# Kernel tuning notes

Measured on AMD Instinct MI355X. Metric: run time of the kernel, lower is better.

## Reference

```python
import jax, jax.numpy as jnp
import numpy as np
from jax.scipy.special import i0

# NUFFT adjoint (gridding) configuration, matching m_op.plan(uv, (256,256), (512,512), (6,6))
N = 256          # image side
K = 512
J = 6            # kernel support per dim
B = 8            # batch
M = 100000       # n_measurements
ALPHA = K / N    # oversampling = 2
BETA = float(np.pi * np.sqrt((J / ALPHA * (ALPHA - 0.5)) ** 2 - 0.8))  # Fessler KB beta


def setup_inputs() -> dict:
    key = jax.random.key(0)
    k1, k2, k3, k4 = jax.random.split(key, 4)
    y_real = jax.random.normal(k1, (B, M), dtype=jnp.float32)
    y_imag = jax.random.normal(k2, (B, M), dtype=jnp.float32)
    weights = jax.random.uniform(k3, (M,), dtype=jnp.float32, minval=0.1, maxval=1.0)
    uv = jax.random.uniform(k4, (M, 2), dtype=jnp.float32,
                            minval=-np.pi, maxval=np.pi)
    return {"y_real": y_real, "y_imag": y_imag, "weights": weights, "uv": uv}


def _kb(t):
    # Kaiser-Bessel interpolation kernel, support |t| <= J/2
    u = 2.0 * t / J
    return i0(BETA * jnp.sqrt(jnp.clip(1.0 - u * u, 0.0))) / i0(jnp.asarray(BETA, jnp.float32))


def reference(y_real, y_imag, weights, uv):
    # weighted complex measurements: inputs * measurement_weights
    y = (y_real + 1j * y_imag) * weights[None, :]           # (B, M) complex64

    # map uv in [-pi, pi) to oversampled grid coords in [0, K)
    kf = uv * (K / (2.0 * np.pi))                            # (M, 2), DC at index 0 (mod K)
    base = jnp.floor(kf).astype(jnp.int32)                   # (M, 2)
    offs = jnp.arange(-J // 2 + 1, J // 2 + 1)               # [-2..3], 6 taps
    idx = base[:, :, None] + offs[None, None, :]             # (M, 2, J)
    dist = idx.astype(jnp.float32) - kf[:, :, None]
    w = _kb(dist)                                            # (M, 2, J) separable weights
    idxm = jnp.mod(idx, K)                                   # wrap onto torus

    w2 = (w[:, 0, :, None] * w[:, 1, None, :]).reshape(M, J * J)          # (M, 36)
    lin = (idxm[:, 0, :, None] * K + idxm[:, 1, None, :]).reshape(M * J * J)
    vals = (y[:, :, None] * w2[None, :, :].astype(jnp.complex64)).reshape(B, M * J * J)

    # scatter-add onto oversampled Fourier grid
    grid = jnp.zeros((B, K * K), jnp.complex64).at[:, lin].add(vals)
    grid = grid.reshape(B, K, K)

    # inverse FFT, center, crop to N x N
    img = jnp.fft.fftshift(jnp.fft.ifft2(grid), axes=(1, 2))
    c = K // 2
    img = img[:, c - N // 2:c + N // 2, c - N // 2:c + N // 2]

    # deapodization: divide by 1D FT of the KB kernel (always real here since BETA > pi*J/4*... )
    n = jnp.arange(N, dtype=jnp.float32) - N // 2
    xf = np.pi * J * n / K
    arg = BETA * BETA - xf * xf
    d = jnp.sinh(jnp.sqrt(arg)) / jnp.sqrt(arg)              # (N,)
    apod = d[:, None] * d[None, :]

    x = (jnp.real(img) / apod).astype(jnp.float32)           # tf.math.real(adj_op(...))

    # per-image min-max rescale
    tmax = jnp.max(x, axis=(1, 2), keepdims=True)
    tmin = jnp.min(x, axis=(1, 2), keepdims=True)
    return (x - tmin) / (tmax - tmin)
```

## Files before the change

### kernel.cpp

```cpp
#include <hip/hip_runtime.h>
#include <math.h>

#define NN 256
#define KK 512
#define JJ 6
#define BB 8
#define MPTS 100000
#define NBINS (KK * KK)
#define KF_SCALE 81.48733086305615f

typedef _Float16 h8 __attribute__((ext_vector_type(8)));
typedef _Float16 h2 __attribute__((ext_vector_type(2)));


__device__ __forceinline__ float i0f_dev(float x) {
    float ax = fabsf(x);
    if (ax < 3.75f) {
        float t = x / 3.75f; t *= t;
        return 1.0f + t*(3.5156229f + t*(3.0899424f + t*(1.2067492f +
               t*(0.2659732f + t*(0.0360768f + t*0.0045813f)))));
    } else {
        float t = 3.75f / ax;
        return (expf(ax) * rsqrtf(ax)) *
               (0.39894228f + t*(0.01328592f + t*(0.00225319f + t*(-0.00157565f +
                t*(0.00916281f + t*(-0.02057706f + t*(0.02635537f +
                t*(-0.01647633f + t*0.00392377f))))))));
    }
}

__device__ __forceinline__ float kbf(float t, float beta, float inv_i0b) {
    float u = t * (1.0f / 3.0f);
    float q = fmaxf(1.0f - u * u, 0.0f);
    return i0f_dev(beta * sqrtf(q)) * inv_i0b;
}

__device__ __forceinline__ int wave_scan(int x, int lane) {
#pragma unroll
    for (int off = 1; off < 64; off <<= 1) {
        int y = __shfl_up(x, off, 64);
        if (lane >= off) x += y;
    }
    return x;
}

__device__ __forceinline__ void build_row_prefix(const int* __restrict__ btot,
                                                 int* sPref, int t)
{
    if (t < 64) {
        int carry = 0;
        if (t == 0) sPref[0] = 0;
#pragma unroll
        for (int k = 0; k < 8; ++k) {
            int x = btot[k * 64 + t];
            int incl = wave_scan(x, t);
            sPref[k * 64 + t + 1] = incl + carry;
            carry += __shfl(incl, 63, 64);
        }
    }
}

__device__ __forceinline__ float kb_lut(const float* __restrict__ sT, float t) {
    float u = (t + 3.0f) * (1023.0f / 6.0f);
    int i = (int)u;
    i = min(i, 1022);
    float f = u - (float)i;
    float a = sT[i];
    return a + f * (sT[i + 1] - sT[i]);
}

__device__ __forceinline__ void tw_lookup(const float* __restrict__ twc,
                                          const float* __restrict__ tws,
                                          int idx, float& wr, float& wi) {
    float sg = (idx & 256) ? -1.0f : 1.0f;
    int ib = idx & 255;
    wr = sg * twc[ib];
    wi = sg * tws[ib];
}


__device__ __forceinline__ void fill_point(
    const float2* __restrict__ uv2,
    const float* __restrict__ y_real, const float* __restrict__ y_imag,
    const float* __restrict__ weights, const int* __restrict__ offsets,
    const int* sPref,
    int* counts, char* rec, const float* sT, int m)
{
    float2 u = uv2[m];
    float kf0 = u.x * KF_SCALE;
    float kf1 = u.y * KF_SCALE;
    float f0 = floorf(kf0), f1 = floorf(kf1);
    float fr0 = kf0 - f0, fr1 = kf1 - f1;
    int b0r = (int)f0 & (KK - 1);
    int b1c = (int)f1 & (KK - 1);
    int bin = (b0r << 9) | b1c;
    int old = atomicSub(&counts[bin], 1);
    int slot = sPref[b0r] + offsets[bin] + old - 1;

    _Float16 hw[12];
#pragma unroll
    for (int j = 0; j < JJ; ++j) {
        hw[j]     = (_Float16)kb_lut(sT, (float)(j - 2) - fr0);
        hw[6 + j] = (_Float16)kb_lut(sT, (float)(j - 2) - fr1);
    }

    float4 c0v, c1v;
    _Float16* p0 = (_Float16*)&c0v;
    _Float16* p1 = (_Float16*)&c1v;
#pragma unroll
    for (int j = 0; j < 8; ++j) p0[j] = hw[j];
#pragma unroll
    for (int j = 0; j < 4; ++j) p1[j] = hw[8 + j];
    ((int*)&c1v)[2] = b1c;
    ((int*)&c1v)[3] = 0;

    float wm = weights[m];
    h8 ha, hb;
#pragma unroll
    for (int b = 0; b < 4; ++b) {
        ha[2 * b]     = (_Float16)(y_real[b * MPTS + m] * wm);
        ha[2 * b + 1] = (_Float16)(y_imag[b * MPTS + m] * wm);
        hb[2 * b]     = (_Float16)(y_real[(b + 4) * MPTS + m] * wm);
        hb[2 * b + 1] = (_Float16)(y_imag[(b + 4) * MPTS + m] * wm);
    }

    float4* dst = (float4*)(rec + (size_t)slot * 64);
    dst[0] = c0v;
    dst[1] = c1v;
    dst[2] = *(float4*)&ha;
    dst[3] = *(float4*)&hb;
}

__device__ __forceinline__ void gather_strip(
    const int* __restrict__ offsets, const int* sPref,
    const char* __restrict__ rec,
    h2* __restrict__ gridh, int j, int w, int lane)
{
    int half = lane >> 5;
    int l32 = lane & 31;
    int xcd = j & 7;
    int c0 = (xcd << 6) + ((j >> 3) & 63);
    int q4 = j >> 9;
    int c1base = (q4 << 7) + (w << 5);
    int c1 = c1base + l32;

    float aR[4], aI[4];
#pragma unroll
    for (int b = 0; b < 4; ++b) { aR[b] = 0.0f; aI[b] = 0.0f; }

    for (int j0 = 0; j0 < JJ; ++j0) {
        int r0 = (c0 - (j0 - 2)) & (KK - 1);
        int rowbase = r0 << 9;
        int P = sPref[r0];
        int rowEnd = sPref[r0 + 1];

        int li = min(lane, 37);
        int vec = offsets[rowbase + ((c1base - 3 + li) & 511)];

        int ps = P + __shfl(vec, l32, 64);
#pragma unroll
        for (int d = 0; d < 6; ++d) {
            int b1 = (c1 - 3 + d) & 511;
            int nxt = P + __shfl(vec, l32 + d + 1, 64);
            int pe = (b1 == 511) ? rowEnd : nxt;
            for (int p = ps; p < pe; ++p) {
                const char* rp = rec + (size_t)p * 64;
                float w0 = (float)*(const _Float16*)(rp + j0 * 2);
                float w1 = (float)*(const _Float16*)(rp + 12 + (5 - d) * 2);
                float ww = w0 * w1;
                h8 yv = *(const h8*)(rp + 32 + (half << 4));
#pragma unroll
                for (int b = 0; b < 4; ++b) {
                    aR[b] += (float)yv[2 * b]     * ww;
                    aI[b] += (float)yv[2 * b + 1] * ww;
                }
            }
            ps = nxt;
        }
    }

    int c = (c0 << 9) + c1;
#pragma unroll
    for (int b = 0; b < 4; ++b) {
        h2 v;
        v[0] = (_Float16)aR[b];
        v[1] = (_Float16)aI[b];
        gridh[((size_t)((half << 2) + b) << 18) + c] = v;
    }
}

__device__ __forceinline__ void wave_fft512(float xr[8], float xi[8], int lane,
                                            const float* __restrict__ twc,
                                            const float* __restrict__ tws)
{
    float a0r = xr[0]+xr[4], a0i = xi[0]+xi[4];
    float a4r = xr[0]-xr[4], a4i = xi[0]-xi[4];
    float a2r = xr[2]+xr[6], a2i = xi[2]+xi[6];
    float a6r = xr[2]-xr[6], a6i = xi[2]-xi[6];
    float a1r = xr[1]+xr[5], a1i = xi[1]+xi[5];
    float a5r = xr[1]-xr[5], a5i = xi[1]-xi[5];
    float a3r = xr[3]+xr[7], a3i = xi[3]+xi[7];
    float a7r = xr[3]-xr[7], a7i = xi[3]-xi[7];
    float b0r = a0r+a2r, b0i = a0i+a2i;
    float b2r = a0r-a2r, b2i = a0i-a2i;
    float b4r = a4r-a6i, b4i = a4i+a6r;
    float b6r = a4r+a6i, b6i = a4i-a6r;
    float b1r = a1r+a3r, b1i = a1i+a3i;
    float b3r = a1r-a3r, b3i = a1i-a3i;
    float b5r = a5r-a7i, b5i = a5i+a7r;
    float b7r = a5r+a7i, b7i = a5i-a7r;
    const float S2 = 0.70710678118654752f;
    float w5r = S2*(b5r-b5i), w5i = S2*(b5r+b5i);
    float w7r = -S2*(b7r+b7i), w7i = S2*(b7r-b7i);
    float y1r = b4r+w5r, y1i = b4i+w5i;
    float y5r = b4r-w5r, y5i = b4i-w5i;
    float y2r = b2r-b3i, y2i = b2i+b3r;
    float y6r = b2r+b3i, y6i = b2i-b3r;
    float y3r = b6r+w7r, y3i = b6i+w7i;
    float y7r = b6r-w7r, y7i = b6i-w7i;

    int p = __brev((unsigned)lane) >> 26;
    xr[0] = b0r+b1r; xi[0] = b0i+b1i;
    {
        float wr, wi;
        tw_lookup(twc, tws, p,     wr, wi); xr[1] = y1r*wr - y1i*wi; xi[1] = y1i*wr + y1r*wi;
        tw_lookup(twc, tws, p * 2, wr, wi); xr[2] = y2r*wr - y2i*wi; xi[2] = y2i*wr + y2r*wi;
        tw_lookup(twc, tws, p * 3, wr, wi); xr[3] = y3r*wr - y3i*wi; xi[3] = y3i*wr + y3r*wi;
        float y4r = b0r-b1r, y4i = b0i-b1i;
        tw_lookup(twc, tws, p * 4, wr, wi); xr[4] = y4r*wr - y4i*wi; xi[4] = y4i*wr + y4r*wi;
        tw_lookup(twc, tws, p * 5, wr, wi); xr[5] = y5r*wr - y5i*wi; xi[5] = y5i*wr + y5r*wi;
        tw_lookup(twc, tws, p * 6, wr, wi); xr[6] = y6r*wr - y6i*wi; xi[6] = y6i*wr + y6r*wi;
        tw_lookup(twc, tws, p * 7, wr, wi); xr[7] = y7r*wr - y7i*wi; xi[7] = y7i*wr + y7r*wi;
    }

#pragma unroll
    for (int t = 0; t < 6; ++t) {
        int m = 1 << t;
        int j = lane & (m - 1);
        int ti = j << (8 - t);
        float wc = twc[ti], wsn = tws[ti];
        bool hi = (lane & m) != 0;
#pragma unroll
        for (int d = 0; d < 8; ++d) {
            float pR = __shfl_xor(xr[d], m, 64);
            float pI = __shfl_xor(xi[d], m, 64);
            float bR = hi ? xr[d] : pR;
            float bI = hi ? xi[d] : pI;
            float aR = hi ? pR : xr[d];
            float aI = hi ? pI : xi[d];
            float wbR = wc * bR - wsn * bI;
            float wbI = wc * bI + wsn * bR;
            xr[d] = hi ? aR - wbR : aR + wbR;
            xi[d] = hi ? aI - wbI : aI + wbI;
        }
    }
}

__device__ __forceinline__ void wave_fft256(float xr[4], float xi[4], int lane,
                                            const float* __restrict__ twc,
                                            const float* __restrict__ tws)
{
    float t0r = xr[0]+xr[2], t0i = xi[0]+xi[2];
    float t1r = xr[0]-xr[2], t1i = xi[0]-xi[2];
    float t2r = xr[1]+xr[3], t2i = xi[1]+xi[3];
    float t3r = xr[1]-xr[3], t3i = xi[1]-xi[3];
    float y1r = t1r-t3i, y1i = t1i+t3r;
    float y3r = t1r+t3i, y3i = t1i-t3r;

    int p2 = (__brev((unsigned)lane) >> 26) << 1;
    xr[0] = t0r+t2r; xi[0] = t0i+t2i;
    {
        float wr, wi;
        tw_lookup(twc, tws, p2,     wr, wi); xr[1] = y1r*wr - y1i*wi; xi[1] = y1i*wr + y1r*wi;
        float y2r = t0r-t2r, y2i = t0i-t2i;
        tw_lookup(twc, tws, p2 * 2, wr, wi); xr[2] = y2r*wr - y2i*wi; xi[2] = y2i*wr + y2r*wi;
        tw_lookup(twc, tws, p2 * 3, wr, wi); xr[3] = y3r*wr - y3i*wi; xi[3] = y3i*wr + y3r*wi;
    }

#pragma unroll
    for (int t = 0; t < 6; ++t) {
        int m = 1 << t;
        int j = lane & (m - 1);
        int ti = j << (8 - t);
        float wc = twc[ti], wsn = tws[ti];
        bool hi = (lane & m) != 0;
#pragma unroll
        for (int d = 0; d < 4; ++d) {
            float pR = __shfl_xor(xr[d], m, 64);
            float pI = __shfl_xor(xi[d], m, 64);
            float bR = hi ? xr[d] : pR;
            float bI = hi ? xi[d] : pI;
            float aR = hi ? pR : xr[d];
            float aI = hi ? pI : xi[d];
            float wbR = wc * bR - wsn * bI;
            float wbI = wc * bI + wsn * bR;
            xr[d] = hi ? aR - wbR : aR + wbR;
            xi[d] = hi ? aI - wbI : aI + wbI;
        }
    }
}

__device__ __forceinline__ void fftA_body(const h2* __restrict__ gridh,
                                          h2* __restrict__ Ch, int bx, int t,
                                          float* sR, float* sI,
                                          float* twc, float* tws)
{
    int lane = t & 63;
    int w = t >> 6;
    int x  = bx & 7;
    int b  = (bx >> 3) & 7;
    int k1base = (x << 6) | (((bx >> 6) & 7) << 3);
    int k1 = k1base + w;

    if (t < 256) {
        float ang = (float)(2.0 * M_PI / 512.0) * (float)t;
        float s, c; sincosf(ang, &s, &c);
        twc[t] = c; tws[t] = s;
    }

    const h2* row = gridh + ((size_t)b << 18) + ((size_t)k1 << 9);
    int p = __brev((unsigned)lane) >> 26;
    float xr[8], xi[8];
#pragma unroll
    for (int a = 0; a < 8; ++a) {
        h2 v = row[p + (a << 6)];
        xr[a] = (float)v[0]; xi[a] = (float)v[1];
    }
    __syncthreads();

    wave_fft512(xr, xi, lane, twc, tws);

    bool act = (lane < 16) | (lane >= 48);
    int lpp = (lane < 16) ? lane : (lane - 32);
    if (act) {
#pragma unroll
        for (int d = 0; d < 8; ++d) {
            int addr = w * 264 + d * 33 + lpp;
            sR[addr] = xr[d];
            sI[addr] = xi[d];
        }
    }
    __syncthreads();

#pragma unroll
    for (int pp = 0; pp < 4; ++pp) {
        int idx = pp * 512 + t;
        int kk = idx & 7;
        int s2 = idx >> 3;
        int v = (s2 + 128) & 255;
        int d = v & 7;
        int lp = v >> 3;
        int addr = kk * 264 + d * 33 + lp;
        h2 o;
        o[0] = (_Float16)sR[addr];
        o[1] = (_Float16)sI[addr];
        Ch[(((size_t)(b << 8) + s2) << 9) + k1base + kk] = o;
    }
}

__device__ __forceinline__ void fftB_body(const h2* __restrict__ Ch,
                                          float* __restrict__ imgT, float beta2,
                                          float* __restrict__ pmin,
                                          float* __restrict__ pmax,
                                          int bx, int t,
                                          float* twc, float* tws, float* invd,
                                          float (*wor)[256], float* wmn, float* wmx)
{
    int lane = t & 63;
    int w = t >> 6;
    int row = w >> 1;
    int odd = w & 1;
    int rowid = bx * 4 + row;
    int b = rowid >> 8;
    int s2 = rowid & 255;

    if (t < 256) {
        float ang = (float)(2.0 * M_PI / 512.0) * (float)t;
        float s, c; sincosf(ang, &s, &c);
        twc[t] = c; tws[t] = s;
    } else if (t < 512) {
        int i = t - 256;
        const float XF = (float)(M_PI * (double)JJ / (double)KK);
        float n = (float)(i - 128);
        float xf = XF * n;
        float arg = beta2 - xf * xf;
        float sq = sqrtf(arg);
        invd[i] = sq / sinhf(sq);
    }

    const h2* rowp = Ch + ((size_t)rowid << 9);
    int p = __brev((unsigned)lane) >> 26;
    float xr[4], xi[4];
#pragma unroll
    for (int a = 0; a < 4; ++a) {
        h2 v = rowp[((p + (a << 6)) << 1) | odd];
        xr[a] = (float)v[0]; xi[a] = (float)v[1];
    }
    __syncthreads();

    wave_fft256(xr, xi, lane, twc, tws);

    if (odd) {
        float4 wo;
#pragma unroll
        for (int d = 0; d < 4; ++d) {
            int k = (lane << 2) + d;
            ((float*)&wo)[d] = xr[d] * twc[k] - xi[d] * tws[k];
        }
        *(float4*)&wor[row][lane << 2] = wo;
    }
    __syncthreads();

    if (!odd) {
        const float INVK2 = 1.0f / ((float)KK * (float)KK);
        float sbase = INVK2 * invd[s2];
        float lmin = 1e30f, lmax = -1e30f;
        float4 wo = *(const float4*)&wor[row][lane << 2];
        float vals[4];
#pragma unroll
        for (int d = 0; d < 4; ++d) {
            int k = (lane << 2) + d;
            float e = xr[d];
            float woK = ((const float*)&wo)[d];
            float xre = (k < 128) ? (e + woK) : (e - woK);
            int r = (k + 128) & 255;
            float o = xre * sbase * invd[r];
            vals[d] = o;
            lmin = fminf(lmin, o);
            lmax = fmaxf(lmax, o);
        }
        int r0run = ((lane << 2) + 128) & 255;
        *(float4*)(imgT + ((size_t)b << 16) + (s2 << 8) + r0run) =
            make_float4(vals[0], vals[1], vals[2], vals[3]);
#pragma unroll
        for (int off = 32; off >= 1; off >>= 1) {
            lmin = fminf(lmin, __shfl_xor(lmin, off, 64));
            lmax = fmaxf(lmax, __shfl_xor(lmax, off, 64));
        }
        if (lane == 0) { wmn[row] = lmin; wmx[row] = lmax; }
    }
    __syncthreads();
    if (t == 0) {
        float mn = fminf(fminf(wmn[0], wmn[1]), fminf(wmn[2], wmn[3]));
        float mx = fmaxf(fmaxf(wmx[0], wmx[1]), fmaxf(wmx[2], wmx[3]));
        pmin[bx] = mn;
        pmax[bx] = mx;
    }
}

__device__ __forceinline__ void norm_body(const float* __restrict__ imgT,
                                          const float* __restrict__ pmin,
                                          const float* __restrict__ pmax,
                                          float* __restrict__ out,
                                          int bx, int t, int nthr,
                                          float (*tile)[65], float* s_mn, float* s_inv)
{
    int b = bx >> 4;
    int tl = bx & 15;
    int r0 = (tl & 3) << 6;
    int s0 = (tl >> 2) << 6;
    int tr = t & 63;
    int ts = t >> 6;
    int nts = nthr >> 6;

    if (t < 64) {
        float mn = pmin[(b << 6) + t];
        float mx = pmax[(b << 6) + t];
#pragma unroll
        for (int off = 32; off >= 1; off >>= 1) {
            mn = fminf(mn, __shfl_xor(mn, off, 64));
            mx = fmaxf(mx, __shfl_xor(mx, off, 64));
        }
        if (t == 0) { *s_mn = mn; *s_inv = 1.0f / (mx - mn); }
    }

    const float* src = imgT + ((size_t)b << 16);
    for (int s2i = ts; s2i < 64; s2i += nts)
        tile[s2i][tr] = src[((s0 + s2i) << 8) + r0 + tr];
    __syncthreads();

    float mn = *s_mn, inv = *s_inv;
    float* dst = out + ((size_t)b << 16);
    for (int ri = ts; ri < 64; ri += nts)
        dst[((r0 + ri) << 8) + s0 + tr] = (tile[tr][ri] - mn) * inv;
}


__global__ __launch_bounds__(256) void count_bins(
    const float2* __restrict__ uv2, int* __restrict__ counts,
    float* __restrict__ lut, float beta, float inv_i0b)
{
    int m = blockIdx.x * 256 + threadIdx.x;
    if (m < 1024) {
        float t = -3.0f + (6.0f / 1023.0f) * (float)m;
        lut[m] = kbf(t, beta, inv_i0b);
    }
    if (m >= MPTS) return;
    float2 u = uv2[m];
    int b0 = (int)floorf(u.x * KF_SCALE) & (KK - 1);
    int b1 = (int)floorf(u.y * KF_SCALE) & (KK - 1);
    atomicAdd(&counts[(b0 << 9) | b1], 1);
}

__global__ __launch_bounds__(512) void scan_a(
    const int* __restrict__ counts, int* __restrict__ offsets,
    int* __restrict__ btot)
{
    __shared__ int part[8];
    int t = threadIdx.x;
    int lane = t & 63;
    int w8 = t >> 6;
    int gid = blockIdx.x * 512 + t;

    int v = counts[gid];
    int x = wave_scan(v, lane);
    if (lane == 63) part[w8] = x;
    __syncthreads();
    if (t < 8) {
        int pq = part[t];
#pragma unroll
        for (int off = 1; off < 8; off <<= 1) {
            int y = __shfl_up(pq, off, 64);
            if (t >= off) pq += y;
        }
        part[t] = pq;
    }
    __syncthreads();
    int incl = x + ((w8 > 0) ? part[w8 - 1] : 0);
    offsets[gid] = incl - v;
    if (t == 511) btot[blockIdx.x] = incl;
}

__global__ __launch_bounds__(256) void fill_records(
    const float2* __restrict__ uv2,
    const float* __restrict__ y_real, const float* __restrict__ y_imag,
    const float* __restrict__ weights, const int* __restrict__ offsets,
    const int* __restrict__ btot,
    int* __restrict__ counts, char* __restrict__ rec,
    const float* __restrict__ lut)
{
    __shared__ float sT[1024];
    __shared__ int sPref[513];
    int tid = threadIdx.x;
#pragma unroll
    for (int q = 0; q < 4; ++q) sT[q * 256 + tid] = lut[q * 256 + tid];
    build_row_prefix(btot, sPref, tid);
    __syncthreads();
    int m = blockIdx.x * 256 + tid;
    if (m >= MPTS) return;
    fill_point(uv2, y_real, y_imag, weights, offsets, sPref, counts, rec, sT, m);
}

__global__ __launch_bounds__(256) void gather_grid(
    const int* __restrict__ offsets, const int* __restrict__ btot,
    const char* __restrict__ rec, h2* __restrict__ gridh)
{
    __shared__ int sPref[513];
    int t = threadIdx.x;
    build_row_prefix(btot, sPref, t);
    __syncthreads();
    gather_strip(offsets, sPref, rec, gridh, blockIdx.x, t >> 6, t & 63);
}

__global__ __launch_bounds__(512) void fftA(
    const h2* __restrict__ gridh, h2* __restrict__ Ch)
{
    __shared__ float sR[2112], sI[2112];
    __shared__ float twc[256], tws[256];
    fftA_body(gridh, Ch, blockIdx.x, threadIdx.x, sR, sI, twc, tws);
}

__global__ __launch_bounds__(512) void fftB(
    const h2* __restrict__ Ch, float* __restrict__ imgT, float beta2,
    float* __restrict__ pmin, float* __restrict__ pmax)
{
    __shared__ float twc[256], tws[256];
    __shared__ float invd[256];
    __shared__ __align__(16) float wor[4][256];
    __shared__ float wmn[4], wmx[4];
    fftB_body(Ch, imgT, beta2, pmin, pmax, blockIdx.x, threadIdx.x,
              twc, tws, invd, wor, wmn, wmx);
}

__global__ __launch_bounds__(256) void norm_t(
    const float* __restrict__ imgT, const float* __restrict__ pmin,
    const float* __restrict__ pmax, float* __restrict__ out)
{
    __shared__ float tile[64][65];
    __shared__ float s_mn, s_inv;
    norm_body(imgT, pmin, pmax, out, blockIdx.x, threadIdx.x, 256,
              tile, &s_mn, &s_inv);
}


static double i0_host(double x) {
    double sum = 1.0, term = 1.0;
    double q = x * x * 0.25;
    for (int k = 1; k < 80; ++k) {
        term *= q / ((double)k * (double)k);
        sum += term;
        if (term < sum * 1e-17) break;
    }
    return sum;
}

extern "C" void kernel_launch(void* const* d_in, const int* in_sizes, int n_in,
                              void* d_out, int out_size, void* d_ws, size_t ws_size,
                              hipStream_t stream)
{
    const float* y_real  = (const float*)d_in[0];
    const float* y_imag  = (const float*)d_in[1];
    const float* weights = (const float*)d_in[2];
    const float2* uv2    = (const float2*)d_in[3];
    float* out = (float*)d_out;

    char* W = (char*)d_ws;
    h2*       gridh   = (h2*)W;
    int*      counts  = (int*)W;
    float*    imgT    = (float*)W;
    char*     A       = W + (size_t)16 * 1024 * 1024;
    char*     rec     = A;
    int*      offsets = (int*)(A + 6400000);
    h2*       Ch      = (h2*)A;
    float*    pmin    = (float*)(A + 8400000);
    float*    pmax    = (float*)(A + 8402048);
    float*    lut     = (float*)(A + 8404096);
    int*      btot    = (int*)(A + 8408192);

    double beta_d = M_PI * sqrt(19.45);
    float beta = (float)beta_d;
    float inv_i0b = (float)(1.0 / i0_host(beta_d));
    float beta2 = (float)(beta_d * beta_d);

    hipMemsetAsync(counts, 0, NBINS * sizeof(int), stream);

    count_bins<<<(MPTS + 255) / 256, 256, 0, stream>>>(
        uv2, counts, lut, beta, inv_i0b);

    scan_a<<<512, 512, 0, stream>>>(counts, offsets, btot);

    fill_records<<<(MPTS + 255) / 256, 256, 0, stream>>>(
        uv2, y_real, y_imag, weights, offsets, btot, counts, rec, lut);

    gather_grid<<<2048, 256, 0, stream>>>(offsets, btot, rec, gridh);

    fftA<<<512, 512, 0, stream>>>(gridh, Ch);

    fftB<<<512, 512, 0, stream>>>(Ch, imgT, beta2, pmin, pmax);

    norm_t<<<128, 256, 0, stream>>>(imgT, pmin, pmax, out);
}
```

Measured before the change: 155.6 us.

## Split gather records into weight/Y arrays and flatten per-row column loops

Splits each 64-byte bin record into separate 32-byte weight and measurement arrays. The gather kernel now preloads offsets and row prefixes for all six rows up front. For non-wrapping columns it walks the six adjacent bins as one contiguous loop, computing the column tap index from comparisons instead of six nested loops. This is meant to cut loop overhead and divergence and to improve load patterns, at the cost of extra compare work per record and more registers.

```diff
diff --git a/kernel.cpp b/kernel.cpp
--- a/kernel.cpp
+++ b/kernel.cpp
@@ -83,7 +83,7 @@
     const float* __restrict__ y_real, const float* __restrict__ y_imag,
     const float* __restrict__ weights, const int* __restrict__ offsets,
     const int* sPref,
-    int* counts, char* rec, const float* sT, int m)
+    int* counts, char* recW, char* recY, const float* sT, int m)
 {
     float2 u = uv2[m];
     float kf0 = u.x * KF_SCALE;
@@ -123,69 +123,12 @@
         hb[2 * b + 1] = (_Float16)(y_imag[(b + 4) * MPTS + m] * wm);
     }
 
-    float4* dst = (float4*)(rec + (size_t)slot * 64);
-    dst[0] = c0v;
-    dst[1] = c1v;
-    dst[2] = *(float4*)&ha;
-    dst[3] = *(float4*)&hb;
-}
-
-__device__ __forceinline__ void gather_strip(
-    const int* __restrict__ offsets, const int* sPref,
-    const char* __restrict__ rec,
-    h2* __restrict__ gridh, int j, int w, int lane)
-{
-    int half = lane >> 5;
-    int l32 = lane & 31;
-    int xcd = j & 7;
-    int c0 = (xcd << 6) + ((j >> 3) & 63);
-    int q4 = j >> 9;
-    int c1base = (q4 << 7) + (w << 5);
-    int c1 = c1base + l32;
-
-    float aR[4], aI[4];
-#pragma unroll
-    for (int b = 0; b < 4; ++b) { aR[b] = 0.0f; aI[b] = 0.0f; }
-
-    for (int j0 = 0; j0 < JJ; ++j0) {
-        int r0 = (c0 - (j0 - 2)) & (KK - 1);
-        int rowbase = r0 << 9;
-        int P = sPref[r0];
-        int rowEnd = sPref[r0 + 1];
-
-        int li = min(lane, 37);
-        int vec = offsets[rowbase + ((c1base - 3 + li) & 511)];
-
-        int ps = P + __shfl(vec, l32, 64);
-#pragma unroll
-        for (int d = 0; d < 6; ++d) {
-            int b1 = (c1 - 3 + d) & 511;
-            int nxt = P + __shfl(vec, l32 + d + 1, 64);
-            int pe = (b1 == 511) ? rowEnd : nxt;
-            for (int p = ps; p < pe; ++p) {
-                const char* rp = rec + (size_t)p * 64;
-                float w0 = (float)*(const _Float16*)(rp + j0 * 2);
-                float w1 = (float)*(const _Float16*)(rp + 12 + (5 - d) * 2);
-                float ww = w0 * w1;
-                h8 yv = *(const h8*)(rp + 32 + (half << 4));
-#pragma unroll
-                for (int b = 0; b < 4; ++b) {
-                    aR[b] += (float)yv[2 * b]     * ww;
-                    aI[b] += (float)yv[2 * b + 1] * ww;
-                }
-            }
-            ps = nxt;
-        }
-    }
-
-    int c = (c0 << 9) + c1;
-#pragma unroll
-    for (int b = 0; b < 4; ++b) {
-        h2 v;
-        v[0] = (_Float16)aR[b];
-        v[1] = (_Float16)aI[b];
-        gridh[((size_t)((half << 2) + b) << 18) + c] = v;
-    }
+    float4* dW = (float4*)(recW + (size_t)slot * 32);
+    dW[0] = c0v;
+    dW[1] = c1v;
+    float4* dY = (float4*)(recY + (size_t)slot * 32);
+    dY[0] = *(float4*)&ha;
+    dY[1] = *(float4*)&hb;
 }
 
 __device__ __forceinline__ void wave_fft512(float xr[8], float xi[8], int lane,
@@ -535,7 +478,7 @@
     const float* __restrict__ y_real, const float* __restrict__ y_imag,
     const float* __restrict__ weights, const int* __restrict__ offsets,
     const int* __restrict__ btot,
-    int* __restrict__ counts, char* __restrict__ rec,
+    int* __restrict__ counts, char* __restrict__ recW, char* __restrict__ recY,
     const float* __restrict__ lut)
 {
     __shared__ float sT[1024];
@@ -547,18 +490,100 @@
     __syncthreads();
     int m = blockIdx.x * 256 + tid;
     if (m >= MPTS) return;
-    fill_point(uv2, y_real, y_imag, weights, offsets, sPref, counts, rec, sT, m);
+    fill_point(uv2, y_real, y_imag, weights, offsets, sPref, counts,
+               recW, recY, sT, m);
 }
 
 __global__ __launch_bounds__(256) void gather_grid(
     const int* __restrict__ offsets, const int* __restrict__ btot,
-    const char* __restrict__ rec, h2* __restrict__ gridh)
+    const char* __restrict__ recW, const char* __restrict__ recY,
+    h2* __restrict__ gridh)
 {
     __shared__ int sPref[513];
     int t = threadIdx.x;
     build_row_prefix(btot, sPref, t);
     __syncthreads();
-    gather_strip(offsets, sPref, rec, gridh, blockIdx.x, t >> 6, t & 63);
+
+    int w = t >> 6;
+    int lane = t & 63;
+    int j = blockIdx.x;
+    int half = lane >> 5;
+    int l32 = lane & 31;
+    int xcd = j & 7;
+    int c0 = (xcd << 6) + ((j >> 3) & 63);
+    int q4 = j >> 9;
+    int c1base = (q4 << 7) + (w << 5);
+    int c1 = c1base + l32;
+    bool lwrap = (c1 < 3) || (c1 >= 509);
+    int li = min(lane, 37);
+
+    float aR[4], aI[4];
+#pragma unroll
+    for (int b = 0; b < 4; ++b) { aR[b] = 0.0f; aI[b] = 0.0f; }
+
+    int vec[6], Pj[6], Ej[6];
+#pragma unroll
+    for (int j0 = 0; j0 < 6; ++j0) {
+        int r0 = (c0 - (j0 - 2)) & (KK - 1);
+        Pj[j0] = sPref[r0];
+        Ej[j0] = sPref[r0 + 1];
+        vec[j0] = offsets[(r0 << 9) + ((c1base - 3 + li) & 511)];
+    }
+
+#pragma unroll
+    for (int j0 = 0; j0 < 6; ++j0) {
+        int P = Pj[j0];
+        int B[7];
+#pragma unroll
+        for (int d = 0; d < 7; ++d)
+            B[d] = P + __shfl(vec[j0], l32 + d, 64);
+
+        if (!lwrap) {
+            for (int p = B[0]; p < B[6]; ++p) {
+                const char* rw = recW + (size_t)p * 32;
+                int dpr = (p >= B[1]) + (p >= B[2]) + (p >= B[3]) +
+                          (p >= B[4]) + (p >= B[5]);
+                float w0 = (float)*(const _Float16*)(rw + j0 * 2);
+                float w1 = (float)*(const _Float16*)(rw + 22 - dpr * 2);
+                float ww = w0 * w1;
+                h8 yv = *(const h8*)(recY + (size_t)p * 32 + (half << 4));
+#pragma unroll
+                for (int b = 0; b < 4; ++b) {
+                    aR[b] += (float)yv[2 * b]     * ww;
+                    aI[b] += (float)yv[2 * b + 1] * ww;
+                }
+            }
+        } else {
+            int rowEnd = Ej[j0];
+            int cm3 = c1 - 3;
+#pragma unroll
+            for (int d = 0; d < 6; ++d) {
+                int col = (cm3 + d) & 511;
+                int ed = (col == 511) ? rowEnd : B[d + 1];
+                for (int p = B[d]; p < ed; ++p) {
+                    const char* rw = recW + (size_t)p * 32;
+                    float w0 = (float)*(const _Float16*)(rw + j0 * 2);
+                    float w1 = (float)*(const _Float16*)(rw + 22 - d * 2);
+                    float ww = w0 * w1;
+                    h8 yv = *(const h8*)(recY + (size_t)p * 32 + (half << 4));
+#pragma unroll
+                    for (int b = 0; b < 4; ++b) {
+                        aR[b] += (float)yv[2 * b]     * ww;
+                        aI[b] += (float)yv[2 * b + 1] * ww;
+                    }
+                }
+            }
+        }
+    }
+
+    int c = (c0 << 9) + c1;
+#pragma unroll
+    for (int b = 0; b < 4; ++b) {
+        h2 v;
+        v[0] = (_Float16)aR[b];
+        v[1] = (_Float16)aI[b];
+        gridh[((size_t)((half << 2) + b) << 18) + c] = v;
+    }
 }
 
 __global__ __launch_bounds__(512) void fftA(
@@ -618,7 +643,8 @@
     int*      counts  = (int*)W;
     float*    imgT    = (float*)W;
     char*     A       = W + (size_t)16 * 1024 * 1024;
-    char*     rec     = A;
+    char*     recW    = A;
+    char*     recY    = A + 3200000;
     int*      offsets = (int*)(A + 6400000);
     h2*       Ch      = (h2*)A;
     float*    pmin    = (float*)(A + 8400000);
@@ -639,9 +665,9 @@
     scan_a<<<512, 512, 0, stream>>>(counts, offsets, btot);
 
     fill_records<<<(MPTS + 255) / 256, 256, 0, stream>>>(
-        uv2, y_real, y_imag, weights, offsets, btot, counts, rec, lut);
-
-    gather_grid<<<2048, 256, 0, stream>>>(offsets, btot, rec, gridh);
+        uv2, y_real, y_imag, weights, offsets, btot, counts, recW, recY, lut);
+
+    gather_grid<<<2048, 256, 0, stream>>>(offsets, btot, recW, recY, gridh);
 
     fftA<<<512, 512, 0, stream>>>(gridh, Ch);
 
```

New measurement: 139.5 us. -10.4%, faster.
